# Kernel tuning notes

Hardware: AMD Instinct MI355X
Metric: run time of the kernel (lower is better)

Reference implementation:

```python
import jax, jax.numpy as jnp
import numpy as np

N = 50000          # node_num
E = 800000         # edges before self-loops (avg degree 16)
H = 1              # heads
C = 64             # out_channel (== embedding dim)
D_IN = 64          # in_channel
NEG_SLOPE = 0.2    # GraphLayer leaky_relu negative_slope
BN_EPS = 1e-5


def setup_inputs() -> dict:
    key = jax.random.key(0)
    ks = jax.random.split(key, 12)
    x = jax.random.normal(ks[0], (N, D_IN), jnp.float32)
    # random edges with no self-loops (forward removes then re-adds self-loops)
    src = jax.random.randint(ks[1], (E,), 0, N, dtype=jnp.int32)
    off = jax.random.randint(ks[2], (E,), 1, N, dtype=jnp.int32)
    dst = (src + off) % N
    edge_index = jnp.stack([src, dst])            # [2, E], row0=j (source), row1=i (target)
    embedding = jax.random.normal(ks[3], (N, C), jnp.float32)
    sc = 1.0 / np.sqrt(D_IN)
    W = jax.random.normal(ks[4], (H * C, D_IN), jnp.float32) * sc   # lin.weight
    att_i = jax.random.normal(ks[5], (1, H, C), jnp.float32) * 0.1
    att_j = jax.random.normal(ks[6], (1, H, C), jnp.float32) * 0.1
    att_em_i = jax.random.normal(ks[7], (1, H, C), jnp.float32) * 0.1
    att_em_j = jax.random.normal(ks[8], (1, H, C), jnp.float32) * 0.1
    bias = jnp.zeros((C,), jnp.float32)           # GraphLayer bias (concat=False)
    bn_gamma = jnp.ones((C,), jnp.float32)
    bn_beta = jnp.zeros((C,), jnp.float32)
    return {"x": x, "edge_index": edge_index, "embedding": embedding, "W": W,
            "att_i": att_i, "att_j": att_j, "att_em_i": att_em_i, "att_em_j": att_em_j,
            "bias": bias, "bn_gamma": bn_gamma, "bn_beta": bn_beta}


def reference(x, edge_index, embedding, W, att_i, att_j, att_em_i, att_em_j, bias, bn_gamma, bn_beta):
    n = x.shape[0]
    xl = (x @ W.T).reshape(n, H, C)                       # lin(x) -> [N, H, C]
    # add self-loops (input edges have none)
    loops = jnp.arange(n, dtype=edge_index.dtype)
    src = jnp.concatenate([edge_index[0], loops])         # j
    dst = jnp.concatenate([edge_index[1], loops])         # i (aggregation target)
    x_j = xl[src]                                         # [E', H, C]
    x_i = xl[dst]
    emb_i = embedding[dst][:, None, :]                    # [E', 1, C] broadcast over heads
    emb_j = embedding[src][:, None, :]
    # alpha = <cat(x_i, emb_i), cat(att_i, att_em_i)> + <cat(x_j, emb_j), cat(att_j, att_em_j)>
    a = ((x_i * att_i).sum(-1) + (emb_i * att_em_i).sum(-1)
         + (x_j * att_j).sum(-1) + (emb_j * att_em_j).sum(-1))   # [E', H]
    a = jnp.where(a >= 0, a, NEG_SLOPE * a)               # leaky_relu(0.2)
    # segment softmax over target nodes
    amax = jax.ops.segment_max(a, dst, num_segments=n)    # every node has a self-loop
    ea = jnp.exp(a - amax[dst])
    denom = jax.ops.segment_sum(ea, dst, num_segments=n)
    alpha = ea / (denom[dst] + 1e-16)                     # [E', H]
    msg = x_j * alpha[..., None]                          # [E', H, C]
    out = jax.ops.segment_sum(msg, dst, num_segments=n)   # [N, H, C]
    out = out.mean(axis=1) + bias                         # concat=False -> head mean
    # BatchNorm1d (training mode: batch stats) + ReLU
    mu = out.mean(axis=0)
    var = ((out - mu) ** 2).mean(axis=0)
    out = (out - mu) * jax.lax.rsqrt(var + BN_EPS) * bn_gamma + bn_beta
    return jnp.maximum(out, 0.0)
```

## Files before the change

kernel.cpp:

```cpp
#include <hip/hip_runtime.h>
#include <hip/hip_bf16.h>

#define NEG_SLOPE 0.2f
#define BN_EPS 1e-5f
#define CAP 48
#define NGRP 391
#define NSLICE 782
#define PER 1024
#define SLICELEN 1024
#define SROW (NGRP + 1)

typedef __attribute__((ext_vector_type(8))) short bf16x8;
typedef __attribute__((ext_vector_type(4))) float f32x4;
typedef __attribute__((ext_vector_type(4))) int i32x4;

__device__ __forceinline__ bf16x8 pk8(float4 a, float4 b) {
    union { __hip_bfloat16 h; short s; } u;
    bf16x8 r;
    u.h = __float2bfloat16(a.x); r[0] = u.s;
    u.h = __float2bfloat16(a.y); r[1] = u.s;
    u.h = __float2bfloat16(a.z); r[2] = u.s;
    u.h = __float2bfloat16(a.w); r[3] = u.s;
    u.h = __float2bfloat16(b.x); r[4] = u.s;
    u.h = __float2bfloat16(b.y); r[5] = u.s;
    u.h = __float2bfloat16(b.z); r[6] = u.s;
    u.h = __float2bfloat16(b.w); r[7] = u.s;
    return r;
}

__device__ __forceinline__ float bf2f(short s) {
    union { __hip_bfloat16 h; short s; } u;
    u.s = s;
    return (float)u.h;
}

__global__ void __launch_bounds__(256, 8)
k_part_mfma(const float* __restrict__ x, const float* __restrict__ W,
            const float* __restrict__ emb,
            const float* __restrict__ att_i, const float* __restrict__ att_j,
            const float* __restrict__ att_em_i, const float* __restrict__ att_em_j,
            const int* __restrict__ src, const int* __restrict__ dst, int E,
            unsigned* __restrict__ region, unsigned short* __restrict__ start16,
            __hip_bfloat16* __restrict__ xlh, float* __restrict__ s_i,
            float* __restrict__ s_j, float* __restrict__ sums, int N) {
    __shared__ unsigned cnt[NGRP];
    __shared__ unsigned pfx[NGRP + 1];
    __shared__ unsigned sbuf[PER];
    int tid = threadIdx.x;
    int lane = tid & 63;
    int m = lane & 15;
    int q = lane >> 4;

    if (blockIdx.x == 0 && tid < 128) sums[tid] = 0.f;

    int gw = blockIdx.x * 4 + (tid >> 6);
    int ntiles = (N + 15) >> 4;
    int r0 = gw * 16;
    int rload = r0 + m; if (rload > N - 1) rload = N - 1;
    const float* xrow = x + (size_t)rload * 64;
    float4 xa0 = *(const float4*)(xrow + q * 8);
    float4 xa1 = *(const float4*)(xrow + q * 8 + 4);
    float4 xb0 = *(const float4*)(xrow + 32 + q * 8);
    float4 xb1 = *(const float4*)(xrow + 32 + q * 8 + 4);

    {
        int b = blockIdx.x;
        int e0 = b * PER;
        int e1 = e0 + PER; if (e1 > E) e1 = E;
        int ecnt = e1 - e0; if (ecnt < 0) ecnt = 0;
        int e4 = ecnt & ~3;
        for (int gg = tid; gg < NGRP; gg += 256) cnt[gg] = 0;
        __syncthreads();
        int o = tid * 4;
        i32x4 d4 = {0, 0, 0, 0}, s4 = d4;
        bool have = o < e4;
        if (have) {
            d4 = *(const i32x4*)(dst + e0 + o);
            s4 = *(const i32x4*)(src + e0 + o);
            atomicAdd(&cnt[d4[0] >> 7], 1u);
            atomicAdd(&cnt[d4[1] >> 7], 1u);
            atomicAdd(&cnt[d4[2] >> 7], 1u);
            atomicAdd(&cnt[d4[3] >> 7], 1u);
        }
        for (int oo = e4 + tid; oo < ecnt; oo += 256)
            atomicAdd(&cnt[dst[e0 + oo] >> 7], 1u);
        __syncthreads();
        if (tid < 64) {
            unsigned loc[7]; unsigned own = 0;
            int g0 = tid * 7;
#pragma unroll
            for (int k = 0; k < 7; ++k) {
                int g = g0 + k;
                unsigned c = (g < NGRP) ? cnt[g] : 0u;
                loc[k] = own; own += c;
            }
            unsigned incl = own;
#pragma unroll
            for (int o2 = 1; o2 < 64; o2 <<= 1) {
                unsigned t = __shfl_up(incl, o2, 64);
                if (tid >= o2) incl += t;
            }
            unsigned excl = incl - own;
#pragma unroll
            for (int k = 0; k < 7; ++k) {
                int g = g0 + k;
                if (g < NGRP) pfx[g] = excl + loc[k];
            }
            if (tid == 0) pfx[NGRP] = (unsigned)ecnt;
        }
        __syncthreads();
        for (int gg = tid; gg < NGRP; gg += 256) cnt[gg] = pfx[gg];
        for (int gg = tid; gg < SROW; gg += 256)
            start16[(size_t)b * SROW + gg] = (unsigned short)pfx[gg];
        __syncthreads();
#define PUT(dd, ss) { int g_ = (dd) >> 7; unsigned p_ = atomicAdd(&cnt[g_], 1u); \
        sbuf[p_] = (((unsigned)((dd) & 127)) << 16) | (unsigned)(ss); }
        if (have) {
            PUT(d4[0], s4[0])
            PUT(d4[1], s4[1])
            PUT(d4[2], s4[2])
            PUT(d4[3], s4[3])
        }
        for (int oo = e4 + tid; oo < ecnt; oo += 256) {
            int d = dst[e0 + oo]; int s = src[e0 + oo];
            PUT(d, s)
        }
#undef PUT
        __syncthreads();
        unsigned* rg = region + (size_t)b * SLICELEN;
        for (int o2 = tid * 4; o2 < ecnt; o2 += 1024)
            *(i32x4*)(rg + o2) = *(const i32x4*)(sbuf + o2);
    }

    if (gw >= ntiles) return;
    bf16x8 A0 = pk8(xa0, xa1);
    bf16x8 A1 = pk8(xb0, xb1);

    f32x4 acc0 = {0.f, 0.f, 0.f, 0.f}, acc1 = acc0, acc2 = acc0, acc3 = acc0;
#define CTILE(ct, accv) { \
        const float* wrow = W + (size_t)(ct * 16 + m) * 64; \
        float4 wb0 = *(const float4*)(wrow + q * 8); \
        float4 wb1 = *(const float4*)(wrow + q * 8 + 4); \
        float4 wb2 = *(const float4*)(wrow + 32 + q * 8); \
        float4 wb3 = *(const float4*)(wrow + 32 + q * 8 + 4); \
        bf16x8 B0 = pk8(wb0, wb1); \
        bf16x8 B1 = pk8(wb2, wb3); \
        accv = __builtin_amdgcn_mfma_f32_16x16x32_bf16(A0, B0, accv, 0, 0, 0); \
        accv = __builtin_amdgcn_mfma_f32_16x16x32_bf16(A1, B1, accv, 0, 0, 0); }
    CTILE(0, acc0) CTILE(1, acc1) CTILE(2, acc2) CTILE(3, acc3)
#undef CTILE

    float ati0 = att_i[m],    ati1 = att_i[16 + m],    ati2 = att_i[32 + m],    ati3 = att_i[48 + m];
    float atj0 = att_j[m],    atj1 = att_j[16 + m],    atj2 = att_j[32 + m],    atj3 = att_j[48 + m];
    float aei0 = att_em_i[m], aei1 = att_em_i[16 + m], aei2 = att_em_i[32 + m], aei3 = att_em_i[48 + m];
    float aej0 = att_em_j[m], aej1 = att_em_j[16 + m], aej2 = att_em_j[32 + m], aej3 = att_em_j[48 + m];
#pragma unroll
    for (int reg = 0; reg < 4; ++reg) {
        int r = r0 + q * 4 + reg;
        if (r < N) {
            float v0 = acc0[reg], v1 = acc1[reg], v2 = acc2[reg], v3 = acc3[reg];
            __hip_bfloat16* xo = xlh + (size_t)r * 64 + m;
            xo[0]  = __float2bfloat16(v0);
            xo[16] = __float2bfloat16(v1);
            xo[32] = __float2bfloat16(v2);
            xo[48] = __float2bfloat16(v3);
            const float* er = emb + (size_t)r * 64 + m;
            float e0 = er[0], e1 = er[16], e2 = er[32], e3 = er[48];
            float pi = v0 * ati0 + v1 * ati1 + v2 * ati2 + v3 * ati3
                     + e0 * aei0 + e1 * aei1 + e2 * aei2 + e3 * aei3;
            float pj = v0 * atj0 + v1 * atj1 + v2 * atj2 + v3 * atj3
                     + e0 * aej0 + e1 * aej1 + e2 * aej2 + e3 * aej3;
#pragma unroll
            for (int o = 1; o < 16; o <<= 1) {
                pi += __shfl_xor(pi, o, 64);
                pj += __shfl_xor(pj, o, 64);
            }
            if (m == 0) { s_i[r] = pi; s_j[r] = pj; }
        }
    }
}

__global__ void __launch_bounds__(512, 4)
k_bucket(const unsigned* __restrict__ region, const unsigned short* __restrict__ start16,
         const float* __restrict__ s_i, const float* __restrict__ s_j,
         uint2* __restrict__ bucket, int* __restrict__ cursor,
         float* __restrict__ denomv, float* __restrict__ wselfv, int N) {
    __shared__ int ldeg[128];
    __shared__ float lsi[128];
    __shared__ float lden[128];
    int tid = threadIdx.x;
    int g = blockIdx.x;
    if (tid < 128) {
        int node = (g << 7) + tid;
        ldeg[tid] = 0;
        float si = 0.f, sj = 0.f;
        if (node < N) { si = s_i[node]; sj = s_j[node]; }
        lsi[tid] = si;
        float a = si + sj;
        a = a >= 0.f ? a : NEG_SLOPE * a;
        float ws = __expf(a);
        lden[tid] = ws;
        if (node < N) wselfv[node] = ws;
    }
    __syncthreads();
    for (int b = tid; b < NSLICE; b += 512) {
        const unsigned short* row = start16 + (size_t)b * SROW + g;
        unsigned st0 = row[0];
        unsigned st1 = row[1];
        const unsigned* rg = region + (size_t)b * SLICELEN;
        for (unsigned i = st0; i < st1; ++i) {
            unsigned e = rg[i];
            int dlo = e >> 16;
            int s = (int)(e & 0xffffu);
            float a = lsi[dlo] + s_j[s];
            a = a >= 0.f ? a : NEG_SLOPE * a;
            float wgt = __expf(a);
            int p = atomicAdd(&ldeg[dlo], 1);
            if (p < CAP) {
                uint2 ent;
                ent.x = (unsigned)s;
                ent.y = __float_as_uint(wgt);
                bucket[((size_t)(g << 7) + dlo) * CAP + p] = ent;
                atomicAdd(&lden[dlo], wgt);
            }
        }
    }
    __syncthreads();
    if (tid < 128) {
        int node = (g << 7) + tid;
        if (node < N) {
            cursor[node] = ldeg[tid];
            denomv[node] = lden[tid] + 1e-16f;
        }
    }
}

__global__ void __launch_bounds__(256, 8)
k_aggregate(const __hip_bfloat16* __restrict__ xlh, const int* __restrict__ cursor,
            const uint2* __restrict__ bucket, const float* __restrict__ denomv,
            const float* __restrict__ wselfv, const float* __restrict__ bias,
            __hip_bfloat16* __restrict__ preh, int N) {
    int lane = threadIdx.x & 63;
    int w = threadIdx.x >> 6;
    int i = blockIdx.x * 4 + w;
    if (i >= N) return;
    int sc = lane & 7;
    int se = lane >> 3;

    size_t base = (size_t)i * CAP;
    uint2 ent = {0u, 0u};
    if (lane < CAP) ent = bucket[base + lane];
    int deg = cursor[i];
    float denom = denomv[i];
    float wself = wselfv[i];
    bf16x8 selfv = *(const bf16x8*)((const short*)xlh + (size_t)i * 64 + sc * 8);

    deg = deg < CAP ? deg : CAP;
    bool valid = lane < deg;
    int jreg = valid ? (int)ent.x : 0;
    float wreg = valid ? __uint_as_float(ent.y) : 0.f;

    float acc8[8];
    float us = (se == 0) ? wself : 0.f;
#pragma unroll
    for (int c = 0; c < 8; ++c) acc8[c] = us * bf2f(selfv[c]);

    int wbits = __float_as_int(wreg);
    int nb8 = (deg + 7) >> 3;
    for (int b = 0; b < nb8; ++b) {
        int e = (b << 3) + se;
        int j = __shfl(jreg, e, 64);
        float u = __int_as_float(__shfl(wbits, e, 64));
        bf16x8 v = *(const bf16x8*)((const short*)xlh + (size_t)j * 64 + sc * 8);
#pragma unroll
        for (int c = 0; c < 8; ++c) acc8[c] = fmaf(u, bf2f(v[c]), acc8[c]);
    }
#pragma unroll
    for (int off = 8; off < 64; off <<= 1) {
#pragma unroll
        for (int c = 0; c < 8; ++c) acc8[c] += __shfl_xor(acc8[c], off, 64);
    }
    if (se == 0) {
        union { __hip_bfloat16 h; short s; } cv;
        bf16x8 r;
#pragma unroll
        for (int c = 0; c < 8; ++c) {
            float rv = acc8[c] / denom + bias[sc * 8 + c];
            cv.h = __float2bfloat16(rv);
            r[c] = cv.s;
        }
        *(bf16x8*)((short*)preh + (size_t)i * 64 + sc * 8) = r;
    }
}

__global__ void k_stats(const __hip_bfloat16* __restrict__ preh, int N,
                        float* __restrict__ sums) {
    int lane = threadIdx.x & 63, w = threadIdx.x >> 6;
    int gwave = blockIdx.x * (blockDim.x >> 6) + w;
    int stride = gridDim.x * (blockDim.x >> 6);
    float s = 0.f, q = 0.f;
    for (int r = gwave; r < N; r += stride) {
        float v = (float)preh[(size_t)r * 64 + lane];
        s += v;
        q = fmaf(v, v, q);
    }
    __shared__ float ls[4][64], lq[4][64];
    ls[w][lane] = s;
    lq[w][lane] = q;
    __syncthreads();
    if (w == 0) {
        s = ls[0][lane] + ls[1][lane] + ls[2][lane] + ls[3][lane];
        q = lq[0][lane] + lq[1][lane] + lq[2][lane] + lq[3][lane];
        atomicAdd(&sums[lane], s);
        atomicAdd(&sums[64 + lane], q);
    }
}

__global__ void __launch_bounds__(256, 4)
k_norm(const __hip_bfloat16* __restrict__ preh, const float* __restrict__ sums,
       const float* __restrict__ gamma, const float* __restrict__ beta,
       float* __restrict__ out, int N, int total4) {
    __shared__ float sc_sh[64], sh_sh[64];
    int tid = threadIdx.x;
    if (tid < 64) {
        float invN = 1.f / (float)N;
        float mu = sums[tid] * invN;
        float var = sums[64 + tid] * invN - mu * mu;
        float sc = gamma[tid] * rsqrtf(var + BN_EPS);
        sc_sh[tid] = sc;
        sh_sh[tid] = beta[tid] - mu * sc;
    }
    __syncthreads();
    typedef __attribute__((ext_vector_type(4))) short s16x4;
    union { s16x4 v; short s[4]; } u;
    for (int i = blockIdx.x * blockDim.x + tid; i < total4; i += gridDim.x * blockDim.x) {
        int c = (i & 15) * 4;
        u.v = ((const s16x4*)preh)[i];
        float4 r;
        union { __hip_bfloat16 h; short s; } cv;
        cv.s = u.s[0]; r.x = fmaxf(fmaf((float)cv.h, sc_sh[c + 0], sh_sh[c + 0]), 0.f);
        cv.s = u.s[1]; r.y = fmaxf(fmaf((float)cv.h, sc_sh[c + 1], sh_sh[c + 1]), 0.f);
        cv.s = u.s[2]; r.z = fmaxf(fmaf((float)cv.h, sc_sh[c + 2], sh_sh[c + 2]), 0.f);
        cv.s = u.s[3]; r.w = fmaxf(fmaf((float)cv.h, sc_sh[c + 3], sh_sh[c + 3]), 0.f);
        ((float4*)out)[i] = r;
    }
}

extern "C" void kernel_launch(void* const* d_in, const int* in_sizes, int n_in,
                              void* d_out, int out_size, void* d_ws, size_t ws_size,
                              hipStream_t stream) {
    const float* x        = (const float*)d_in[0];
    const int*   ei       = (const int*)d_in[1];
    const float* emb      = (const float*)d_in[2];
    const float* W        = (const float*)d_in[3];
    const float* att_i    = (const float*)d_in[4];
    const float* att_j    = (const float*)d_in[5];
    const float* att_em_i = (const float*)d_in[6];
    const float* att_em_j = (const float*)d_in[7];
    const float* bias     = (const float*)d_in[8];
    const float* gamma    = (const float*)d_in[9];
    const float* beta     = (const float*)d_in[10];

    int N = in_sizes[0] / 64;
    int E = in_sizes[1] / 2;
    const int* srcv = ei;
    const int* dstv = ei + E;

    char* ws = (char*)d_ws;
    size_t o = 0;
    auto alloc = [&](size_t bytes) -> char* {
        char* p = ws + o;
        o += bytes;
        o = (o + 255) & ~(size_t)255;
        return p;
    };
    __hip_bfloat16* xlh     = (__hip_bfloat16*)alloc((size_t)N * 64 * 2);
    __hip_bfloat16* preh    = (__hip_bfloat16*)alloc((size_t)N * 64 * 2);
    float* s_i              = (float*)alloc((size_t)N * 4);
    float* s_j              = (float*)alloc((size_t)N * 4);
    uint2* bucket           = (uint2*)alloc((size_t)N * CAP * 8);
    int* cursor             = (int*)alloc((size_t)N * 4);
    float* denomv           = (float*)alloc((size_t)N * 4);
    float* wselfv           = (float*)alloc((size_t)N * 4);
    unsigned* region        = (unsigned*)alloc((size_t)NSLICE * SLICELEN * 4);
    unsigned short* start16 = (unsigned short*)alloc((size_t)NSLICE * SROW * 2);
    float* sums             = (float*)alloc(128 * 4);

    int nslice = (E + PER - 1) / PER;
    k_part_mfma<<<nslice, 256, 0, stream>>>(x, W, emb, att_i, att_j, att_em_i,
                                            att_em_j, srcv, dstv, E, region, start16,
                                            xlh, s_i, s_j, sums, N);
    k_bucket<<<NGRP, 512, 0, stream>>>(region, start16, s_i, s_j, bucket, cursor,
                                       denomv, wselfv, N);
    k_aggregate<<<(N + 3) / 4, 256, 0, stream>>>(xlh, cursor, bucket, denomv,
                                                 wselfv, bias, preh, N);
    k_stats<<<256, 256, 0, stream>>>(preh, N, sums);
    int total4 = N * 16;
    k_norm<<<1024, 256, 0, stream>>>(preh, sums, gamma, beta, (float*)d_out, N, total4);
}
```

Measured before the change: 165.2 us.

## Fuse bucketing, aggregation and BN stats into one LDS-accumulating kernel

Replaces the bucket, aggregate and stats kernels with one kernel per 128-node group. The kernel accumulates weighted source features directly into a 128x64 fp32 LDS tile using shared-memory atomics, and load-balances edges across threads with a prefix-scan over slice counts plus a binary search. It then computes the per-channel BN partial sums in the same pass. This removes the intermediate bucket buffer, the degree cap and two kernel launches, at the cost of 64 LDS atomics per edge, only 391 blocks running, and large LDS use that limits occupancy.

```diff
diff --git a/kernel.cpp b/kernel.cpp
--- a/kernel.cpp
+++ b/kernel.cpp
@@ -3,7 +3,6 @@
 
 #define NEG_SLOPE 0.2f
 #define BN_EPS 1e-5f
-#define CAP 48
 #define NGRP 391
 #define NSLICE 782
 #define PER 1024
@@ -181,138 +180,134 @@
 }
 
 __global__ void __launch_bounds__(512, 4)
-k_bucket(const unsigned* __restrict__ region, const unsigned short* __restrict__ start16,
-         const float* __restrict__ s_i, const float* __restrict__ s_j,
-         uint2* __restrict__ bucket, int* __restrict__ cursor,
-         float* __restrict__ denomv, float* __restrict__ wselfv, int N) {
-    __shared__ int ldeg[128];
+k_bucket_agg(const unsigned* __restrict__ region,
+             const unsigned short* __restrict__ start16,
+             const float* __restrict__ s_i, const float* __restrict__ s_j,
+             const __hip_bfloat16* __restrict__ xlh, const float* __restrict__ bias,
+             __hip_bfloat16* __restrict__ preh, float* __restrict__ sums, int N) {
+    __shared__ float lnum[128][64];
+    __shared__ float lden[128];
     __shared__ float lsi[128];
-    __shared__ float lden[128];
+    __shared__ float wsl[128];
+    __shared__ unsigned soff[NSLICE + 1];
+    __shared__ unsigned short sst[NSLICE];
+    __shared__ float lsum[64], lsq[64];
+    __shared__ int wcur;
     int tid = threadIdx.x;
     int g = blockIdx.x;
+
+    if (tid == 0) wcur = 0;
+    if (tid < 64) { lsum[tid] = 0.f; lsq[tid] = 0.f; }
     if (tid < 128) {
         int node = (g << 7) + tid;
-        ldeg[tid] = 0;
         float si = 0.f, sj = 0.f;
         if (node < N) { si = s_i[node]; sj = s_j[node]; }
         lsi[tid] = si;
         float a = si + sj;
         a = a >= 0.f ? a : NEG_SLOPE * a;
         float ws = __expf(a);
+        wsl[tid] = ws;
         lden[tid] = ws;
-        if (node < N) wselfv[node] = ws;
-    }
-    __syncthreads();
+    }
+    for (int k = tid; k < 128 * 64; k += 512) ((float*)lnum)[k] = 0.f;
     for (int b = tid; b < NSLICE; b += 512) {
-        const unsigned short* row = start16 + (size_t)b * SROW + g;
-        unsigned st0 = row[0];
-        unsigned st1 = row[1];
-        const unsigned* rg = region + (size_t)b * SLICELEN;
-        for (unsigned i = st0; i < st1; ++i) {
-            unsigned e = rg[i];
+        unsigned st0 = start16[(size_t)b * SROW + g];
+        unsigned st1 = start16[(size_t)b * SROW + g + 1];
+        sst[b] = (unsigned short)st0;
+        soff[b] = st1 - st0;
+    }
+    __syncthreads();
+    if (tid < 64) {
+        unsigned loc[13]; unsigned own = 0;
+        int b0 = tid * 13;
+#pragma unroll
+        for (int k = 0; k < 13; ++k) {
+            int b = b0 + k;
+            unsigned c = (b < NSLICE) ? soff[b] : 0u;
+            loc[k] = own; own += c;
+        }
+        unsigned incl = own;
+#pragma unroll
+        for (int o = 1; o < 64; o <<= 1) {
+            unsigned t = __shfl_up(incl, o, 64);
+            if (tid >= o) incl += t;
+        }
+        unsigned excl = incl - own;
+#pragma unroll
+        for (int k = 0; k < 13; ++k) {
+            int b = b0 + k;
+            if (b < NSLICE) soff[b] = excl + loc[k];
+        }
+        if (tid == 63) soff[NSLICE] = incl;
+    }
+    __syncthreads();
+    int tot = (int)soff[NSLICE];
+    for (;;) {
+        int k0 = atomicAdd(&wcur, 2);
+        if (k0 >= tot) break;
+        int kend = k0 + 2 < tot ? k0 + 2 : tot;
+        for (int k = k0; k < kend; ++k) {
+            int lo = 0, hi = NSLICE;
+            while (hi - lo > 1) {
+                int mid = (lo + hi) >> 1;
+                if (soff[mid] <= (unsigned)k) lo = mid; else hi = mid;
+            }
+            unsigned e = region[(size_t)lo * SLICELEN + sst[lo] + ((unsigned)k - soff[lo])];
             int dlo = e >> 16;
             int s = (int)(e & 0xffffu);
             float a = lsi[dlo] + s_j[s];
             a = a >= 0.f ? a : NEG_SLOPE * a;
             float wgt = __expf(a);
-            int p = atomicAdd(&ldeg[dlo], 1);
-            if (p < CAP) {
-                uint2 ent;
-                ent.x = (unsigned)s;
-                ent.y = __float_as_uint(wgt);
-                bucket[((size_t)(g << 7) + dlo) * CAP + p] = ent;
-                atomicAdd(&lden[dlo], wgt);
-            }
-        }
-    }
-    __syncthreads();
-    if (tid < 128) {
-        int node = (g << 7) + tid;
+            atomicAdd(&lden[dlo], wgt);
+            const bf16x8* row = (const bf16x8*)((const short*)xlh + (size_t)s * 64);
+            float* nrow = lnum[dlo];
+#pragma unroll
+            for (int o = 0; o < 8; ++o) {
+                bf16x8 v = row[o];
+#pragma unroll
+                for (int c = 0; c < 8; ++c)
+                    atomicAdd(&nrow[o * 8 + c], wgt * bf2f(v[c]));
+            }
+        }
+    }
+    __syncthreads();
+    {
+        int nl = tid >> 2;
+        int c0 = (tid & 3) * 16;
+        int node = (g << 7) + nl;
         if (node < N) {
-            cursor[node] = ldeg[tid];
-            denomv[node] = lden[tid] + 1e-16f;
-        }
-    }
-}
-
-__global__ void __launch_bounds__(256, 8)
-k_aggregate(const __hip_bfloat16* __restrict__ xlh, const int* __restrict__ cursor,
-            const uint2* __restrict__ bucket, const float* __restrict__ denomv,
-            const float* __restrict__ wselfv, const float* __restrict__ bias,
-            __hip_bfloat16* __restrict__ preh, int N) {
-    int lane = threadIdx.x & 63;
-    int w = threadIdx.x >> 6;
-    int i = blockIdx.x * 4 + w;
-    if (i >= N) return;
-    int sc = lane & 7;
-    int se = lane >> 3;
-
-    size_t base = (size_t)i * CAP;
-    uint2 ent = {0u, 0u};
-    if (lane < CAP) ent = bucket[base + lane];
-    int deg = cursor[i];
-    float denom = denomv[i];
-    float wself = wselfv[i];
-    bf16x8 selfv = *(const bf16x8*)((const short*)xlh + (size_t)i * 64 + sc * 8);
-
-    deg = deg < CAP ? deg : CAP;
-    bool valid = lane < deg;
-    int jreg = valid ? (int)ent.x : 0;
-    float wreg = valid ? __uint_as_float(ent.y) : 0.f;
-
-    float acc8[8];
-    float us = (se == 0) ? wself : 0.f;
-#pragma unroll
-    for (int c = 0; c < 8; ++c) acc8[c] = us * bf2f(selfv[c]);
-
-    int wbits = __float_as_int(wreg);
-    int nb8 = (deg + 7) >> 3;
-    for (int b = 0; b < nb8; ++b) {
-        int e = (b << 3) + se;
-        int j = __shfl(jreg, e, 64);
-        float u = __int_as_float(__shfl(wbits, e, 64));
-        bf16x8 v = *(const bf16x8*)((const short*)xlh + (size_t)j * 64 + sc * 8);
-#pragma unroll
-        for (int c = 0; c < 8; ++c) acc8[c] = fmaf(u, bf2f(v[c]), acc8[c]);
-    }
-#pragma unroll
-    for (int off = 8; off < 64; off <<= 1) {
-#pragma unroll
-        for (int c = 0; c < 8; ++c) acc8[c] += __shfl_xor(acc8[c], off, 64);
-    }
-    if (se == 0) {
-        union { __hip_bfloat16 h; short s; } cv;
-        bf16x8 r;
-#pragma unroll
-        for (int c = 0; c < 8; ++c) {
-            float rv = acc8[c] / denom + bias[sc * 8 + c];
-            cv.h = __float2bfloat16(rv);
-            r[c] = cv.s;
-        }
-        *(bf16x8*)((short*)preh + (size_t)i * 64 + sc * 8) = r;
-    }
-}
-
-__global__ void k_stats(const __hip_bfloat16* __restrict__ preh, int N,
-                        float* __restrict__ sums) {
-    int lane = threadIdx.x & 63, w = threadIdx.x >> 6;
-    int gwave = blockIdx.x * (blockDim.x >> 6) + w;
-    int stride = gridDim.x * (blockDim.x >> 6);
-    float s = 0.f, q = 0.f;
-    for (int r = gwave; r < N; r += stride) {
-        float v = (float)preh[(size_t)r * 64 + lane];
-        s += v;
-        q = fmaf(v, v, q);
-    }
-    __shared__ float ls[4][64], lq[4][64];
-    ls[w][lane] = s;
-    lq[w][lane] = q;
-    __syncthreads();
-    if (w == 0) {
-        s = ls[0][lane] + ls[1][lane] + ls[2][lane] + ls[3][lane];
-        q = lq[0][lane] + lq[1][lane] + lq[2][lane] + lq[3][lane];
-        atomicAdd(&sums[lane], s);
-        atomicAdd(&sums[64 + lane], q);
+            float den = lden[nl] + 1e-16f;
+            float ws = wsl[nl];
+            const short* xr = (const short*)xlh + (size_t)node * 64 + c0;
+            bf16x8 x0 = *(const bf16x8*)xr;
+            bf16x8 x1 = *(const bf16x8*)(xr + 8);
+            union { __hip_bfloat16 h; short s; } cv;
+            bf16x8 o0, o1;
+#pragma unroll
+            for (int c = 0; c < 8; ++c) {
+                float rv = (lnum[nl][c0 + c] + ws * bf2f(x0[c])) / den + bias[c0 + c];
+                cv.h = __float2bfloat16(rv); o0[c] = cv.s;
+                float rq = (float)cv.h;
+                atomicAdd(&lsum[c0 + c], rq);
+                atomicAdd(&lsq[c0 + c], rq * rq);
+            }
+#pragma unroll
+            for (int c = 0; c < 8; ++c) {
+                float rv = (lnum[nl][c0 + 8 + c] + ws * bf2f(x1[c])) / den + bias[c0 + 8 + c];
+                cv.h = __float2bfloat16(rv); o1[c] = cv.s;
+                float rq = (float)cv.h;
+                atomicAdd(&lsum[c0 + 8 + c], rq);
+                atomicAdd(&lsq[c0 + 8 + c], rq * rq);
+            }
+            short* pr = (short*)preh + (size_t)node * 64 + c0;
+            *(bf16x8*)pr = o0;
+            *(bf16x8*)(pr + 8) = o1;
+        }
+    }
+    __syncthreads();
+    if (tid < 64) {
+        atomicAdd(&sums[tid], lsum[tid]);
+        atomicAdd(&sums[64 + tid], lsq[tid]);
     }
 }
 
@@ -378,10 +373,6 @@
     __hip_bfloat16* preh    = (__hip_bfloat16*)alloc((size_t)N * 64 * 2);
     float* s_i              = (float*)alloc((size_t)N * 4);
     float* s_j              = (float*)alloc((size_t)N * 4);
-    uint2* bucket           = (uint2*)alloc((size_t)N * CAP * 8);
-    int* cursor             = (int*)alloc((size_t)N * 4);
-    float* denomv           = (float*)alloc((size_t)N * 4);
-    float* wselfv           = (float*)alloc((size_t)N * 4);
     unsigned* region        = (unsigned*)alloc((size_t)NSLICE * SLICELEN * 4);
     unsigned short* start16 = (unsigned short*)alloc((size_t)NSLICE * SROW * 2);
     float* sums             = (float*)alloc(128 * 4);
@@ -390,11 +381,8 @@
     k_part_mfma<<<nslice, 256, 0, stream>>>(x, W, emb, att_i, att_j, att_em_i,
                                             att_em_j, srcv, dstv, E, region, start16,
                                             xlh, s_i, s_j, sums, N);
-    k_bucket<<<NGRP, 512, 0, stream>>>(region, start16, s_i, s_j, bucket, cursor,
-                                       denomv, wselfv, N);
-    k_aggregate<<<(N + 3) / 4, 256, 0, stream>>>(xlh, cursor, bucket, denomv,
-                                                 wselfv, bias, preh, N);
-    k_stats<<<256, 256, 0, stream>>>(preh, N, sums);
+    k_bucket_agg<<<NGRP, 512, 0, stream>>>(region, start16, s_i, s_j, xlh,
+                                           bias, preh, sums, N);
     int total4 = N * 16;
     k_norm<<<1024, 256, 0, stream>>>(preh, sums, gamma, beta, (float*)d_out, N, total4);
 }
```

New measurement: 507.4 us. +207.1%, slower.
